# Kernel tuning notes

Measured on AMD Instinct MI355X. Metric: run time of the kernel, lower is better.

The kernel has to match this reference:

```python
import jax, jax.numpy as jnp
import numpy as np
from jax import lax

T = 8        # num_frames
EPS = 1e-5   # batchnorm eps


def conv2d(x, w, b=None, pad=0):
    y = lax.conv_general_dilated(x, w, (1, 1), [(pad, pad), (pad, pad)],
                                 dimension_numbers=('NCHW', 'OIHW', 'NCHW'))
    return y if b is None else y + b[None, :, None, None]


def conv3d(x, w, b, pad=1):
    y = lax.conv_general_dilated(x, w, (1, 1, 1), [(pad, pad)] * 3,
                                 dimension_numbers=('NCDHW', 'OIDHW', 'NCDHW'))
    return y + b[None, :, None, None, None]


def bn(x, g, b, m, v):
    shp = (1, -1) + (1,) * (x.ndim - 2)
    return (x - m.reshape(shp)) * (g.reshape(shp) * lax.rsqrt(v.reshape(shp) + EPS)) + b.reshape(shp)


def deform_conv2d(x, offset, weight, pad):
    # mmcv DeformConv: x (N,C,H,W); offset (N,2*kh*kw,H,W) laid out as (tap, [dy,dx]);
    # weight (O,C,kh,kw); stride 1, zero padding outside sampled via masked bilinear.
    N, C, H, W = x.shape
    O, _, kh, kw = weight.shape
    K = kh * kw
    off = offset.reshape(N, K, 2, H, W)
    ky, kx = jnp.meshgrid(jnp.arange(kh), jnp.arange(kw), indexing='ij')
    # fractional sample coords per (n, tap, out_y, out_x)
    py = (jnp.arange(H)[None, :, None] + (ky.reshape(K) - pad)[:, None, None])[None] + off[:, :, 0]
    px = (jnp.arange(W)[None, None, :] + (kx.reshape(K) - pad)[:, None, None])[None] + off[:, :, 1]
    y0 = jnp.floor(py); x0 = jnp.floor(px)
    ly = py - y0;       lx = px - x0
    y0 = y0.astype(jnp.int32); x0 = x0.astype(jnp.int32)
    xf = x.reshape(N, C, H * W)

    def gather(iy, ix):
        valid = ((iy >= 0) & (iy < H) & (ix >= 0) & (ix < W)).astype(x.dtype)
        lin = jnp.clip(iy, 0, H - 1) * W + jnp.clip(ix, 0, W - 1)   # (N,K,H,W)
        v = jax.vmap(lambda xi, li: xi[:, li])(xf, lin)             # (N,C,K,H,W)
        return v * valid[:, None]

    val = (gather(y0, x0)         * ((1 - ly) * (1 - lx))[:, None]
           + gather(y0, x0 + 1)   * ((1 - ly) * lx)[:, None]
           + gather(y0 + 1, x0)   * (ly * (1 - lx))[:, None]
           + gather(y0 + 1, x0 + 1) * (ly * lx)[:, None])
    return jnp.einsum('nckhw,ock->nohw', val, weight.reshape(O, C, K))


def reference(x, w_down, b_down, bn1_g, bn1_b, bn1_m, bn1_v,
              tconv_w, tconv_b, bnt_g, bnt_b, bnt_m, bnt_v,
              off3_w, off3_b, def3_w, off5_w, off5_b, def5_w,
              conv1_w, conv1_b, bn3_g, bn3_b, bn3_m, bn3_v,
              conv_w, conv_b, bn2_g, bn2_b, bn2_m, bn2_v):
    out = bn(conv2d(x, w_down, b_down), bn1_g, bn1_b, bn1_m, bn1_v)   # (nt, cr, h, w)
    nt, cr, h, w = out.shape
    b = nt // T
    # temporal branch: (b, cr, T, h, w) 3D conv, then mean over time
    t_in = out.reshape(b, T, cr, h, w).transpose(0, 2, 1, 3, 4)
    t_out = bn(conv3d(t_in, tconv_w, tconv_b), bnt_g, bnt_b, bnt_m, bnt_v)
    t_out = t_out.mean(axis=2, keepdims=True).transpose(0, 2, 1, 3, 4)  # (b,1,cr,h,w)
    # motion-difference branches
    o5 = out.reshape(b, T, cr, h, w)
    x_pre = o5[:, :T - 1]
    x_post = o5[:, 1:].reshape(-1, cr, h, w)                           # (b*(T-1), cr, h, w)
    d3 = deform_conv2d(x_post, conv2d(x_post, off3_w, off3_b, pad=1), def3_w, pad=1).reshape(b, T - 1, cr, h, w)
    d5 = deform_conv2d(x_post, conv2d(x_post, off5_w, off5_b, pad=2), def5_w, pad=2).reshape(b, T - 1, cr, h, w)
    mp = lax.reduce_window(x_post, -jnp.inf, lax.max, (1, 1, 3, 3), (1, 1, 1, 1),
                           [(0, 0), (0, 0), (1, 1), (1, 1)])
    d_avg = bn(conv2d(mp, conv1_w, conv1_b), bn3_g, bn3_b, bn3_m, bn3_v).reshape(b, T - 1, cr, h, w)
    diff = jnp.abs(d3 + d5 + d_avg - 3.0 * x_pre)                      # (d3-pre)+(d5-pre)+(avg-pre)
    cat = jnp.concatenate([diff, t_out], axis=1).reshape(-1, cr, h, w) # (nt, cr, h, w)
    gate = bn(conv2d(cat.mean(axis=(2, 3), keepdims=True), conv_w, conv_b),
              bn2_g, bn2_b, bn2_m, bn2_v)
    gate = jax.nn.sigmoid(gate) - 0.5
    return gate * x + x


def setup_inputs():
    key = jax.random.key(0)
    ks = iter(jax.random.split(key, 64))
    C, CR, H, W, B = 256, 64, 28, 28, 8
    NT = B * T
    rn = lambda shape, s: jax.random.normal(next(ks), shape, jnp.float32) * s

    def bnp(c):
        return (1.0 + rn((c,), 0.1), rn((c,), 0.1), rn((c,), 0.1),
                0.5 + jax.random.uniform(next(ks), (c,), jnp.float32))

    inp = {'x': rn((NT, C, H, W), 1.0)}
    inp['w_down'] = rn((CR, C, 1, 1), 0.06); inp['b_down'] = rn((CR,), 0.02)
    inp['bn1_g'], inp['bn1_b'], inp['bn1_m'], inp['bn1_v'] = bnp(CR)
    inp['tconv_w'] = rn((CR, CR, 3, 3, 3), 0.024); inp['tconv_b'] = rn((CR,), 0.02)
    inp['bnt_g'], inp['bnt_b'], inp['bnt_m'], inp['bnt_v'] = bnp(CR)
    inp['off3_w'] = rn((18, CR, 3, 3), 0.01); inp['off3_b'] = rn((18,), 0.01)
    inp['def3_w'] = rn((CR, CR, 3, 3), 0.04)
    inp['off5_w'] = rn((50, CR, 5, 5), 0.005); inp['off5_b'] = rn((50,), 0.01)
    inp['def5_w'] = rn((CR, CR, 5, 5), 0.025)
    inp['conv1_w'] = rn((CR, CR, 1, 1), 0.125); inp['conv1_b'] = rn((CR,), 0.02)
    inp['bn3_g'], inp['bn3_b'], inp['bn3_m'], inp['bn3_v'] = bnp(CR)
    inp['conv_w'] = rn((C, CR, 1, 1), 0.125); inp['conv_b'] = rn((C,), 0.02)
    inp['bn2_g'], inp['bn2_b'], inp['bn2_m'], inp['bn2_v'] = bnp(C)
    return inp
```

## Files before the change

kernel.cpp:

```cpp
#include <hip/hip_runtime.h>
#include <hip/hip_bf16.h>

#define HW 784
#define WD 28
#define NPX (56 * 784)
#define PLANE (56 * 64 * 784)
#define PADPX 1024

using short8 = __attribute__((ext_vector_type(8))) short;
using f32x4  = __attribute__((ext_vector_type(4))) float;

__device__ __forceinline__ float b2f(short s)
{
  return __uint_as_float(((unsigned)(unsigned short)s) << 16);
}

__global__ void k_prep(
    const float* __restrict__ w_down, const float* __restrict__ b_down,
    const float* __restrict__ bn1_g, const float* __restrict__ bn1_b,
    const float* __restrict__ bn1_m, const float* __restrict__ bn1_v,
    const float* __restrict__ tconv_w, const float* __restrict__ tconv_b,
    const float* __restrict__ bnt_g, const float* __restrict__ bnt_b,
    const float* __restrict__ bnt_m, const float* __restrict__ bnt_v,
    const float* __restrict__ off3_w, const float* __restrict__ def3_w,
    const float* __restrict__ off5_w, const float* __restrict__ def5_w,
    const float* __restrict__ conv1_w, const float* __restrict__ conv1_b,
    const float* __restrict__ bn3_g, const float* __restrict__ bn3_b,
    const float* __restrict__ bn3_m, const float* __restrict__ bn3_v,
    const float* __restrict__ conv_w, const float* __restrict__ conv_b,
    const float* __restrict__ bn2_g, const float* __restrict__ bn2_b,
    const float* __restrict__ bn2_m, const float* __restrict__ bn2_v,
    __hip_bfloat16* __restrict__ wdB, float* __restrict__ bias1,
    float* __restrict__ wtT, float* __restrict__ AtBt,
    __hip_bfloat16* __restrict__ wBs3, __hip_bfloat16* __restrict__ wBs5,
    __hip_bfloat16* __restrict__ wBd, __hip_bfloat16* __restrict__ c1B,
    float* __restrict__ B3,
    float* __restrict__ gwT, float* __restrict__ Bg)
{
  const int tid = blockIdx.x * blockDim.x + threadIdx.x;
  const int nth = gridDim.x * blockDim.x;
  for (int i = tid; i < 16 * 4 * 512; i += nth) {
    int j = i & 7; int lane = (i >> 3) & 63;
    int rest = i >> 9; int nt = rest & 3; int ch = rest >> 2;
    int c = (ch & 7) * 32 + ((lane >> 4) << 3) + j;
    int oc = nt * 16 + (lane & 15);
    float s = bn1_g[oc] / sqrtf(bn1_v[oc] + 1e-5f);
    float wv = w_down[oc * 256 + c] * s;
    __hip_bfloat16 h = __float2bfloat16(wv);
    float hi = b2f(*(short*)&h);
    wdB[i] = (ch < 8) ? h : __float2bfloat16(wv - hi);
  }
  for (int i = tid; i < 64; i += nth) {
    float s = bn1_g[i] / sqrtf(bn1_v[i] + 1e-5f);
    bias1[i] = (b_down[i] - bn1_m[i]) * s + bn1_b[i];
  }
  for (int i = tid; i < 192 * 9 * 64; i += nth) {
    int cc = i / (9 * 64); int tap = (i / 64) % 9; int o = i & 63;
    int dt = cc >> 6, c = cc & 63;
    wtT[i] = tconv_w[o * 1728 + c * 27 + dt * 9 + tap];
  }
  for (int i = tid; i < 64; i += nth) {
    float s = bnt_g[i] / sqrtf(bnt_v[i] + 1e-5f);
    AtBt[i] = s * 0.125f;
    AtBt[64 + i] = (tconv_b[i] - bnt_m[i]) * s + bnt_b[i];
  }
  for (int i = tid; i < 9 * 2 * 2 * 512; i += nth) {
    int j = i & 7; int lane = (i >> 3) & 63;
    int rest = i >> 9; int nt = rest % 2; rest /= 2;
    int chunk = rest & 1; int tap = rest >> 1;
    int c = chunk * 32 + ((lane >> 4) << 3) + j;
    int oc = nt * 16 + (lane & 15);
    float v = (oc < 18) ? off3_w[oc * 576 + c * 9 + tap] : 0.f;
    wBs3[i] = __float2bfloat16(v);
  }
  for (int i = tid; i < 25 * 2 * 4 * 512; i += nth) {
    int j = i & 7; int lane = (i >> 3) & 63;
    int rest = i >> 9; int nt = rest % 4; rest /= 4;
    int chunk = rest & 1; int tap = rest >> 1;
    int c = chunk * 32 + ((lane >> 4) << 3) + j;
    int oc = nt * 16 + (lane & 15);
    float v = (oc < 50) ? off5_w[oc * 1600 + c * 25 + tap] : 0.f;
    wBs5[i] = __float2bfloat16(v);
  }
  for (int i = tid; i < 34 * 2 * 4 * 512; i += nth) {
    int j = i & 7; int lane = (i >> 3) & 63;
    int rest = i >> 9; int nt = rest & 3; rest >>= 2;
    int chunk = rest & 1; int tap = rest >> 1;
    int c = chunk * 32 + ((lane >> 4) << 3) + j;
    int oc = nt * 16 + (lane & 15);
    float v = (tap < 9) ? def3_w[oc * 576 + c * 9 + tap]
                        : def5_w[oc * 1600 + c * 25 + (tap - 9)];
    wBd[i] = __float2bfloat16(v);
  }
  for (int i = tid; i < 2 * 4 * 512; i += nth) {
    int j = i & 7; int lane = (i >> 3) & 63;
    int rest = i >> 9; int nt = rest & 3; int chunk = rest >> 2;
    int c = chunk * 32 + ((lane >> 4) << 3) + j;
    int oc = nt * 16 + (lane & 15);
    float s = bn3_g[oc] / sqrtf(bn3_v[oc] + 1e-5f);
    c1B[i] = __float2bfloat16(conv1_w[oc * 64 + c] * s);
  }
  for (int i = tid; i < 64; i += nth) {
    float s = bn3_g[i] / sqrtf(bn3_v[i] + 1e-5f);
    B3[i] = (conv1_b[i] - bn3_m[i]) * s + bn3_b[i];
  }
  for (int i = tid; i < 64 * 256; i += nth) {
    int c = i >> 8, co = i & 255;
    float s = bn2_g[co] / sqrtf(bn2_v[co] + 1e-5f);
    gwT[i] = conv_w[co * 64 + c] * s;
  }
  for (int i = tid; i < 256; i += nth) {
    float s = bn2_g[i] / sqrtf(bn2_v[i] + 1e-5f);
    Bg[i] = (conv_b[i] - bn2_m[i]) * s + bn2_b[i];
  }
}

__global__ void k_zerohalo(float4* __restrict__ p)
{
  const int i = blockIdx.x * 256 + threadIdx.x;
  const int n = i / 1920, rem = i % 1920;
  const int sl = rem >> 3, q = rem & 7;
  int row, col;
  if (sl < 128) {
    int r = sl >> 5;
    row = (r & 1) + ((r >> 1) * 30);
    col = sl & 31;
  } else {
    int t2 = sl - 128;
    row = 2 + (t2 >> 2);
    int qq = t2 & 3;
    col = (qq & 1) + ((qq >> 1) * 30);
  }
  p[((size_t)n * 1024 + row * 32 + col) * 8 + q] =
      make_float4(0.f, 0.f, 0.f, 0.f);
}

__global__ __launch_bounds__(256) void k_down(
    const float* __restrict__ x, const __hip_bfloat16* __restrict__ wdB,
    const float* __restrict__ bias1, float* __restrict__ out,
    __hip_bfloat16* __restrict__ xTbP)
{
  __shared__ float ct[64 * 65];
  const int tid = threadIdx.x;
  const int w = tid >> 6, lane = tid & 63;
  const int quad = lane >> 4, mrow = lane & 15;
  const int gpx = blockIdx.x * 64 + w * 16 + mrow;
  const int f = gpx / HW, px = gpx % HW;
  const float* xp = x + (size_t)f * 256 * HW + px;
  f32x4 acc[4];
#pragma unroll
  for (int nt = 0; nt < 4; nt++) acc[nt] = (f32x4){0.f, 0.f, 0.f, 0.f};

#pragma unroll
  for (int ch = 0; ch < 8; ch++) {
    short8 aH, aL;
#pragma unroll
    for (int j = 0; j < 8; j++) {
      float xv = xp[(ch * 32 + quad * 8 + j) * HW];
      __hip_bfloat16 h = __float2bfloat16(xv);
      aH[j] = *(short*)&h;
      __hip_bfloat16 l = __float2bfloat16(xv - b2f(aH[j]));
      aL[j] = *(short*)&l;
    }
    const short* bwH = (const short*)wdB + (size_t)(ch * 4) * 512 + lane * 8;
    const short* bwL = bwH + 16384;
#pragma unroll
    for (int nt = 0; nt < 4; nt++) {
      short8 bH = *(const short8*)(bwH + nt * 512);
      short8 bL = *(const short8*)(bwL + nt * 512);
      acc[nt] = __builtin_amdgcn_mfma_f32_16x16x32_bf16(aH, bH, acc[nt], 0, 0, 0);
      acc[nt] = __builtin_amdgcn_mfma_f32_16x16x32_bf16(aL, bH, acc[nt], 0, 0, 0);
      acc[nt] = __builtin_amdgcn_mfma_f32_16x16x32_bf16(aH, bL, acc[nt], 0, 0, 0);
    }
  }
#pragma unroll
  for (int nt = 0; nt < 4; nt++) {
    int oc_l = nt * 16 + mrow;
#pragma unroll
    for (int reg = 0; reg < 4; reg++)
      ct[oc_l * 65 + w * 16 + quad * 4 + reg] = acc[nt][reg];
  }
  __syncthreads();
  for (int i = tid; i < 4096; i += 256) {
    int oc = i >> 6, p2 = i & 63;
    int g2 = blockIdx.x * 64 + p2;
    int f2 = g2 / HW, px2 = g2 % HW;
    out[((size_t)f2 * 64 + oc) * HW + px2] = ct[oc * 65 + p2] + bias1[oc];
  }
  for (int i = tid; i < 4096; i += 256) {
    int p2 = i >> 6, oc = i & 63;
    int g2 = blockIdx.x * 64 + p2;
    int f2 = g2 / HW, px2 = g2 % HW;
    if (f2 & 7) {
      int n = (f2 >> 3) * 7 + (f2 & 7) - 1;
      int py = px2 / WD, pxc = px2 % WD;
      __hip_bfloat16 q = __float2bfloat16(ct[oc * 65 + p2] + bias1[oc]);
      ((short*)xTbP)[((size_t)n * PADPX + (py + 2) * 32 + (pxc + 2)) * 64 + oc] =
          *(short*)&q;
    }
  }
}

__global__ void k_makeU(const float* __restrict__ out, float* __restrict__ U)
{
  const int idx = blockIdx.x * 256 + threadIdx.x;
  const int b = idx / (64 * HW);
  const int r = idx % (64 * HW);
  const float* p = out + (size_t)b * 8 * 64 * HW + r;
  float v0 = p[0];
  float s = v0, v = v0;
#pragma unroll
  for (int t = 1; t < 8; t++) { v = p[t * 64 * HW]; s += v; }
  float* u = U + (size_t)b * 192 * HW + r;
  u[0] = s - v;
  u[64 * HW] = s;
  u[128 * HW] = s - v0;
}

__global__ __launch_bounds__(256) void k_tconv(
    const float* __restrict__ U, const float* __restrict__ wtT,
    const float* __restrict__ AtBt, float* __restrict__ t_out)
{
  __shared__ float wl[16 * 9 * 4];
  const int tid = threadIdx.x;
  const int b = blockIdx.x;
  const int px = blockIdx.y * 256 + tid;
  const int o0 = blockIdx.z * 4;
  const bool act = px < HW;
  const int pxe = act ? px : 0;
  const int y = pxe / WD, x = pxe % WD;
  int lin[9]; float msk[9];
#pragma unroll
  for (int t = 0; t < 9; t++) {
    int iy = y + t / 3 - 1, ix = x + t % 3 - 1;
    bool ok = iy >= 0 && iy < WD && ix >= 0 && ix < WD;
    lin[t] = min(max(iy, 0), WD - 1) * WD + min(max(ix, 0), WD - 1);
    msk[t] = ok ? 1.f : 0.f;
  }
  float acc[4];
#pragma unroll
  for (int j = 0; j < 4; j++) acc[j] = 0.f;
  const float* ub = U + (size_t)b * 192 * HW;
  for (int ccb = 0; ccb < 12; ccb++) {
    __syncthreads();
    for (int i = tid; i < 576; i += 256) {
      int ccL = i / 36; int rr = i % 36; int tap = rr >> 2; int j = rr & 3;
      wl[i] = wtT[((ccb * 16 + ccL) * 9 + tap) * 64 + o0 + j];
    }
    __syncthreads();
    for (int ccL = 0; ccL < 16; ccL++) {
      const float* p = ub + (ccb * 16 + ccL) * HW;
      float v[9];
#pragma unroll
      for (int t = 0; t < 9; t++) v[t] = p[lin[t]] * msk[t];
      const float* wr = &wl[ccL * 36];
#pragma unroll
      for (int t = 0; t < 9; t++)
#pragma unroll
        for (int j = 0; j < 4; j++) acc[j] += v[t] * wr[t * 4 + j];
    }
  }
  if (act) {
#pragma unroll
    for (int j = 0; j < 4; j++) {
      int o = o0 + j;
      t_out[(size_t)(b * 64 + o) * HW + px] = acc[j] * AtBt[o] + AtBt[64 + o];
    }
  }
}

template <int KS, int PAD, int OC, int NT>
__global__ __launch_bounds__(256) void k_offconv_mfma(
    const __hip_bfloat16* __restrict__ xTbP,
    const __hip_bfloat16* __restrict__ wBs,
    const float* __restrict__ bias, float* __restrict__ dst)
{
  constexpr int K2 = KS * KS;
  __shared__ float ct[NT * 16 * 65];
  const int tid = threadIdx.x;
  const int w = tid >> 6, lane = tid & 63;
  const int quad = lane >> 4, mrow = lane & 15;
  const int gpx = blockIdx.x * 64 + w * 16 + mrow;
  const int n = gpx / HW, px = gpx % HW;
  const int y = px / WD, x = px % WD;
  const short* xb = (const short*)xTbP + ((size_t)n * PADPX) * 64;
  f32x4 acc[NT];
#pragma unroll
  for (int nt = 0; nt < NT; nt++) acc[nt] = (f32x4){0.f, 0.f, 0.f, 0.f};

  for (int tap = 0; tap < K2; tap++) {
    const short* bw = (const short*)wBs + (size_t)tap * NT * 1024 + lane * 8;
    short8 bf[2 * NT];
#pragma unroll
    for (int q = 0; q < 2 * NT; q++) bf[q] = *(const short8*)(bw + q * 512);
    int ty = tap / KS, tx = tap % KS;
    int sp = (y + ty + (2 - PAD)) * 32 + (x + tx + (2 - PAD));
    const short* ap = xb + sp * 64 + quad * 8;
    short8 a0 = *(const short8*)(ap);
    short8 a1 = *(const short8*)(ap + 32);
#pragma unroll
    for (int nt = 0; nt < NT; nt++)
      acc[nt] = __builtin_amdgcn_mfma_f32_16x16x32_bf16(a0, bf[nt], acc[nt], 0, 0, 0);
#pragma unroll
    for (int nt = 0; nt < NT; nt++)
      acc[nt] = __builtin_amdgcn_mfma_f32_16x16x32_bf16(a1, bf[NT + nt], acc[nt], 0, 0, 0);
  }
#pragma unroll
  for (int nt = 0; nt < NT; nt++) {
    int oc_l = nt * 16 + mrow;
#pragma unroll
    for (int reg = 0; reg < 4; reg++) {
      int pxr = w * 16 + quad * 4 + reg;
      ct[oc_l * 65 + pxr] = acc[nt][reg];
    }
  }
  __syncthreads();
  for (int i = tid; i < OC * 64; i += 256) {
    int oc = i >> 6, p2 = i & 63;
    int g2 = blockIdx.x * 64 + p2;
    int n2 = g2 / HW, px2 = g2 % HW;
    dst[((size_t)n2 * OC + oc) * HW + px2] = ct[oc * 65 + p2] + bias[oc];
  }
}

__global__ __launch_bounds__(448, 6) void k_deform_mfma(
    const __hip_bfloat16* __restrict__ xTbP,
    const float* __restrict__ off3b, const float* __restrict__ off5b,
    const __hip_bfloat16* __restrict__ wBd,
    float* __restrict__ dsum, float* __restrict__ pext)
{
  __shared__ __align__(128) short Fr[784 * 32];
  const int tid = threadIdx.x;
  const int w = tid >> 6, lane = tid & 63;
  const int quad = lane >> 4, mrow = lane & 15;
  const int part = blockIdx.x, n = blockIdx.y, csel = blockIdx.z;

  {
    const short* xb = (const short*)xTbP + (size_t)n * PADPX * 64;
    for (int idx = tid; idx < 784 * 4; idx += 448) {
      int px = idx >> 2, s = idx & 3;
      int py = px / WD, pxc = px % WD;
      float4 v = ((const float4*)(xb + ((py + 2) * 32 + (pxc + 2)) * 64))[csel * 4 + s];
      int slot = (px & ~1) * 4 + ((s ^ ((px >> 1) & 3)) << 1) + (px & 1);
      ((float4*)Fr)[slot] = v;
    }
  }
  __syncthreads();

  const char* F = (const char*)Fr;
  const int px0 = (part * 7 + w) * 16;
  const int pxg = px0 + mrow;
  const int y_g = pxg / WD, x_g = pxg % WD;
  const float* ob3 = off3b + (size_t)n * 18 * HW + pxg;
  const float* ob5 = off5b + (size_t)n * 50 * HW + pxg;

  f32x4 acc[4];
#pragma unroll
  for (int nt = 0; nt < 4; nt++) acc[nt] = (f32x4){0.f, 0.f, 0.f, 0.f};

#pragma unroll 2
  for (int tap = 0; tap < 34; tap++) {
    const short* bw = (const short*)wBd +
        ((size_t)(tap * 2 + csel) * 4) * 512 + lane * 8;
    short8 bfrag[4];
#pragma unroll
    for (int nt = 0; nt < 4; nt++) bfrag[nt] = *(const short8*)(bw + nt * 512);

    int kk, ty, tx, PADl; const float* obp;
    if (tap < 9) { kk = tap; ty = kk / 3; tx = kk % 3; PADl = 1; obp = ob3; }
    else { kk = tap - 9; ty = kk / 5; tx = kk % 5; PADl = 2; obp = ob5; }
    float offy = obp[(2 * kk) * HW];
    float offx = obp[(2 * kk + 1) * HW];
    float py = (float)(y_g + ty - PADl) + offy;
    float pxx = (float)(x_g + tx - PADl) + offx;
    float fy = floorf(py), fx = floorf(pxx);
    int y0 = (int)fy, x0 = (int)fx;
    float ly = py - fy, lx = pxx - fx;
    int y1 = y0 + 1, x1 = x0 + 1;
    float vy0 = (y0 >= 0 && y0 < WD) ? 1.f : 0.f;
    float vy1 = (y1 >= 0 && y1 < WD) ? 1.f : 0.f;
    float vx0 = (x0 >= 0 && x0 < WD) ? 1.f : 0.f;
    float vx1 = (x1 >= 0 && x1 < WD) ? 1.f : 0.f;
    float w00 = (1.f - ly) * (1.f - lx) * vy0 * vx0;
    float w01 = (1.f - ly) * lx * vy0 * vx1;
    float w10 = ly * (1.f - lx) * vy1 * vx0;
    float w11 = ly * lx * vy1 * vx1;
    int cy0 = min(max(y0, 0), WD - 1), cy1 = min(max(y1, 0), WD - 1);
    int cx0 = min(max(x0, 0), WD - 1), cx1 = min(max(x1, 0), WD - 1);
    int r00 = cy0 * WD + cx0, r01 = cy0 * WD + cx1;
    int r10 = cy1 * WD + cx0, r11 = cy1 * WD + cx1;
#define LADDR(r) ((r & ~1) * 64 + (((quad ^ ((r >> 1) & 3))) << 5) + ((r & 1) << 4))
    short8 c00 = *(const short8*)(F + LADDR(r00));
    short8 c01 = *(const short8*)(F + LADDR(r01));
    short8 c10 = *(const short8*)(F + LADDR(r10));
    short8 c11 = *(const short8*)(F + LADDR(r11));
#undef LADDR
    short8 a0;
#pragma unroll
    for (int j = 0; j < 8; j++) {
      float g0 = b2f(c00[j]) * w00 + b2f(c01[j]) * w01 +
                 b2f(c10[j]) * w10 + b2f(c11[j]) * w11;
      __hip_bfloat16 q0 = __float2bfloat16(g0);
      a0[j] = *(short*)&q0;
    }
#pragma unroll
    for (int nt = 0; nt < 4; nt++)
      acc[nt] = __builtin_amdgcn_mfma_f32_16x16x32_bf16(a0, bfrag[nt], acc[nt], 0, 0, 0);
  }

  float* P = csel ? pext : dsum;
#pragma unroll
  for (int nt = 0; nt < 4; nt++)
    *(f32x4*)(P + ((size_t)n * 64 + nt * 16 + mrow) * HW + px0 + quad * 4) =
        acc[nt];
}

__global__ __launch_bounds__(256) void k_davg_diff(
    const float* __restrict__ frames, const __hip_bfloat16* __restrict__ c1B,
    const float* __restrict__ B3, float* __restrict__ dsum,
    const float* __restrict__ pext)
{
  const int tid = threadIdx.x;
  const int w = tid >> 6, lane = tid & 63;
  const int quad = lane >> 4, mrow = lane & 15;
  const int gpx = blockIdx.x * 64 + w * 16 + mrow;
  const int n = gpx / HW, px = gpx % HW;
  const int fpost = (n / 7) * 8 + (n % 7) + 1;
  const int fpre = fpost - 1;
  const int y = px / WD, x = px % WD;
  int lin[9]; bool okm[9];
#pragma unroll
  for (int t2 = 0; t2 < 9; t2++) {
    int iy = y + t2 / 3 - 1, ix = x + t2 % 3 - 1;
    okm[t2] = iy >= 0 && iy < WD && ix >= 0 && ix < WD;
    lin[t2] = min(max(iy, 0), WD - 1) * WD + min(max(ix, 0), WD - 1);
  }
  const float* sb = frames + (size_t)fpost * 64 * HW;
  f32x4 acc[4];
#pragma unroll
  for (int nt = 0; nt < 4; nt++) acc[nt] = (f32x4){0.f, 0.f, 0.f, 0.f};

#pragma unroll
  for (int chunk = 0; chunk < 2; chunk++) {
    short8 aM;
#pragma unroll
    for (int j = 0; j < 8; j++) {
      const float* p = sb + (chunk * 32 + quad * 8 + j) * HW;
      float m = -1e30f;
#pragma unroll
      for (int t2 = 0; t2 < 9; t2++) {
        float v = okm[t2] ? p[lin[t2]] : -1e30f;
        m = fmaxf(m, v);
      }
      __hip_bfloat16 h = __float2bfloat16(m);
      aM[j] = *(short*)&h;
    }
    const short* bw = (const short*)c1B + (size_t)(chunk * 4) * 512 + lane * 8;
#pragma unroll
    for (int nt = 0; nt < 4; nt++) {
      short8 bf = *(const short8*)(bw + nt * 512);
      acc[nt] = __builtin_amdgcn_mfma_f32_16x16x32_bf16(aM, bf, acc[nt], 0, 0, 0);
    }
  }
  const int pxb = (px - mrow) + quad * 4;
#pragma unroll
  for (int nt = 0; nt < 4; nt++) {
    int oc = nt * 16 + mrow;
    size_t base = ((size_t)n * 64 + oc) * HW + pxb;
    f32x4 ds = *(const f32x4*)(dsum + base);
    f32x4 pe = *(const f32x4*)(pext + base);
    f32x4 xp4 = *(const f32x4*)(frames + ((size_t)fpre * 64 + oc) * HW + pxb);
    float b3 = B3[oc];
    f32x4 o;
#pragma unroll
    for (int r = 0; r < 4; r++)
      o[r] = fabsf(ds[r] + pe[r] + acc[nt][r] + b3 - 3.f * xp4[r]);
    *(f32x4*)(dsum + base) = o;
  }
}

__global__ __launch_bounds__(256) void k_gmean(
    const float* __restrict__ dsum, const float* __restrict__ t_out,
    float* __restrict__ gmean)
{
  const int nt = blockIdx.x, cg = blockIdx.y;
  const int c = cg * 4 + (threadIdx.x >> 6), lane = threadIdx.x & 63;
  const int b = nt >> 3, tt = nt & 7;
  const float* p = (tt < 7) ? (dsum + (size_t)((b * 7 + tt) * 64 + c) * HW)
                            : (t_out + (size_t)(b * 64 + c) * HW);
  float s = 0.f;
  for (int i = lane; i < HW; i += 64) s += p[i];
#pragma unroll
  for (int o = 32; o > 0; o >>= 1) s += __shfl_down(s, o, 64);
  if (lane == 0) gmean[nt * 64 + c] = s * (1.f / HW);
}

__global__ __launch_bounds__(256) void k_gate(
    const float* __restrict__ gmean, const float* __restrict__ gwT,
    const float* __restrict__ Bg, float* __restrict__ mult)
{
  __shared__ float gm[64];
  const int nt = blockIdx.x, co = threadIdx.x;
  if (co < 64) gm[co] = gmean[nt * 64 + co];
  __syncthreads();
  float a = 0.f;
#pragma unroll 8
  for (int c = 0; c < 64; c++) a += gm[c] * gwT[c * 256 + co];
  float pre = a + Bg[co];
  mult[nt * 256 + co] = 0.5f + 1.f / (1.f + expf(-pre));
}

__global__ void k_apply(const float* __restrict__ x,
                        const float* __restrict__ mult,
                        float* __restrict__ outp)
{
  const int i = blockIdx.x * 256 + threadIdx.x;
  const int plane = i / 196;
  const float m = mult[plane];
  float4 v = ((const float4*)x)[i];
  v.x *= m; v.y *= m; v.z *= m; v.w *= m;
  ((float4*)outp)[i] = v;
}

extern "C" void kernel_launch(void* const* d_in, const int* in_sizes, int n_in,
                              void* d_out, int out_size, void* d_ws, size_t ws_size,
                              hipStream_t stream)
{
  const float* x       = (const float*)d_in[0];
  const float* w_down  = (const float*)d_in[1];
  const float* b_down  = (const float*)d_in[2];
  const float* bn1_g   = (const float*)d_in[3];
  const float* bn1_b   = (const float*)d_in[4];
  const float* bn1_m   = (const float*)d_in[5];
  const float* bn1_v   = (const float*)d_in[6];
  const float* tconv_w = (const float*)d_in[7];
  const float* tconv_b = (const float*)d_in[8];
  const float* bnt_g   = (const float*)d_in[9];
  const float* bnt_b   = (const float*)d_in[10];
  const float* bnt_m   = (const float*)d_in[11];
  const float* bnt_v   = (const float*)d_in[12];
  const float* off3_w  = (const float*)d_in[13];
  const float* off3_b  = (const float*)d_in[14];
  const float* def3_w  = (const float*)d_in[15];
  const float* off5_w  = (const float*)d_in[16];
  const float* off5_b  = (const float*)d_in[17];
  const float* def5_w  = (const float*)d_in[18];
  const float* conv1_w = (const float*)d_in[19];
  const float* conv1_b = (const float*)d_in[20];
  const float* bn3_g   = (const float*)d_in[21];
  const float* bn3_b   = (const float*)d_in[22];
  const float* bn3_m   = (const float*)d_in[23];
  const float* bn3_v   = (const float*)d_in[24];
  const float* conv_w  = (const float*)d_in[25];
  const float* conv_b  = (const float*)d_in[26];
  const float* bn2_g   = (const float*)d_in[27];
  const float* bn2_b   = (const float*)d_in[28];
  const float* bn2_m   = (const float*)d_in[29];
  const float* bn2_v   = (const float*)d_in[30];

  float* ws = (float*)d_ws;
  float* out_b  = ws; ws += 64 * 64 * HW;
  float* U      = ws; ws += 8 * 192 * HW;
  float* t_out  = ws; ws += 8 * 64 * HW;
  float* off3b  = ws; ws += 56 * 18 * HW;
  float* off5b  = ws; ws += 56 * 50 * HW;
  float* dsum   = ws; ws += PLANE;
  float* pext   = ws; ws += PLANE;
  float* gmean  = ws; ws += 64 * 64;
  float* multb  = ws; ws += 64 * 256;
  float* bias1  = ws; ws += 64;
  float* wtT    = ws; ws += 192 * 9 * 64;
  float* AtBt   = ws; ws += 128;
  float* B3     = ws; ws += 64;
  float* gwT    = ws; ws += 64 * 256;
  float* Bg     = ws; ws += 256;
  __hip_bfloat16* wdB  = (__hip_bfloat16*)ws; ws += 16384;
  __hip_bfloat16* wBs3 = (__hip_bfloat16*)ws; ws += 9216;
  __hip_bfloat16* wBs5 = (__hip_bfloat16*)ws; ws += 51200;
  __hip_bfloat16* wBd  = (__hip_bfloat16*)ws; ws += 69632;
  __hip_bfloat16* c1B  = (__hip_bfloat16*)ws; ws += 2048;
  __hip_bfloat16* xTbP = (__hip_bfloat16*)ws; ws += 56 * PADPX * 64 / 2;

  k_prep<<<256, 256, 0, stream>>>(
      w_down, b_down, bn1_g, bn1_b, bn1_m, bn1_v,
      tconv_w, tconv_b, bnt_g, bnt_b, bnt_m, bnt_v,
      off3_w, def3_w, off5_w, def5_w,
      conv1_w, conv1_b, bn3_g, bn3_b, bn3_m, bn3_v,
      conv_w, conv_b, bn2_g, bn2_b, bn2_m, bn2_v,
      wdB, bias1, wtT, AtBt, wBs3, wBs5, wBd, c1B,
      B3, gwT, Bg);
  k_zerohalo<<<420, 256, 0, stream>>>((float4*)xTbP);

  k_down<<<784, 256, 0, stream>>>(x, wdB, bias1, out_b, xTbP);
  k_makeU<<<1568, 256, 0, stream>>>(out_b, U);
  k_tconv<<<dim3(8, 4, 16), 256, 0, stream>>>(U, wtT, AtBt, t_out);
  k_offconv_mfma<3, 1, 18, 2><<<686, 256, 0, stream>>>(xTbP, wBs3, off3_b, off3b);
  k_offconv_mfma<5, 2, 50, 4><<<686, 256, 0, stream>>>(xTbP, wBs5, off5_b, off5b);
  k_deform_mfma<<<dim3(7, 56, 2), 448, 0, stream>>>(xTbP, off3b, off5b, wBd,
                                                    dsum, pext);
  k_davg_diff<<<686, 256, 0, stream>>>(out_b, c1B, B3, dsum, pext);
  k_gmean<<<dim3(64, 16), 256, 0, stream>>>(dsum, t_out, gmean);
  k_gate<<<64, 256, 0, stream>>>(gmean, gwT, Bg, multb);
  k_apply<<<12544, 256, 0, stream>>>(x, multb, (float*)d_out);
}
```

Before: 403.5 us.

## Compute temporal conv mean via border-masked row sums and fuse gmean into diff kernel

The full 3D temporal conv output was only consumed through its spatial mean, so it is replaced by per-channel 3x3 border-masked window sums (k_rsum) contracted with the weights in a tiny k_tmean kernel. The separate U construction, the tconv kernel and the gmean reduction pass are removed. The davg_diff kernel now reduces its absolute differences directly into gacc with atomics instead of writing them out. The deform kernel's LDS swizzle is also simplified. Atomic float accumulation makes summation order nondeterministic.

```diff
diff --git a/kernel.cpp b/kernel.cpp
--- a/kernel.cpp
+++ b/kernel.cpp
@@ -35,10 +35,12 @@
     __hip_bfloat16* __restrict__ wBs3, __hip_bfloat16* __restrict__ wBs5,
     __hip_bfloat16* __restrict__ wBd, __hip_bfloat16* __restrict__ c1B,
     float* __restrict__ B3,
-    float* __restrict__ gwT, float* __restrict__ Bg)
+    float* __restrict__ gwT, float* __restrict__ Bg,
+    float* __restrict__ gacc)
 {
   const int tid = blockIdx.x * blockDim.x + threadIdx.x;
   const int nth = gridDim.x * blockDim.x;
+  for (int i = tid; i < 64 * 64; i += nth) gacc[i] = 0.f;
   for (int i = tid; i < 16 * 4 * 512; i += nth) {
     int j = i & 7; int lane = (i >> 3) & 63;
     int rest = i >> 9; int nt = rest & 3; int ch = rest >> 2;
@@ -201,71 +203,67 @@
   }
 }
 
-__global__ void k_makeU(const float* __restrict__ out, float* __restrict__ U)
-{
-  const int idx = blockIdx.x * 256 + threadIdx.x;
-  const int b = idx / (64 * HW);
-  const int r = idx % (64 * HW);
-  const float* p = out + (size_t)b * 8 * 64 * HW + r;
-  float v0 = p[0];
-  float s = v0, v = v0;
-#pragma unroll
-  for (int t = 1; t < 8; t++) { v = p[t * 64 * HW]; s += v; }
-  float* u = U + (size_t)b * 192 * HW + r;
-  u[0] = s - v;
-  u[64 * HW] = s;
-  u[128 * HW] = s - v0;
-}
-
-__global__ __launch_bounds__(256) void k_tconv(
-    const float* __restrict__ U, const float* __restrict__ wtT,
-    const float* __restrict__ AtBt, float* __restrict__ t_out)
-{
-  __shared__ float wl[16 * 9 * 4];
-  const int tid = threadIdx.x;
-  const int b = blockIdx.x;
-  const int px = blockIdx.y * 256 + tid;
-  const int o0 = blockIdx.z * 4;
-  const bool act = px < HW;
-  const int pxe = act ? px : 0;
-  const int y = pxe / WD, x = pxe % WD;
-  int lin[9]; float msk[9];
-#pragma unroll
-  for (int t = 0; t < 9; t++) {
-    int iy = y + t / 3 - 1, ix = x + t % 3 - 1;
-    bool ok = iy >= 0 && iy < WD && ix >= 0 && ix < WD;
-    lin[t] = min(max(iy, 0), WD - 1) * WD + min(max(ix, 0), WD - 1);
-    msk[t] = ok ? 1.f : 0.f;
-  }
-  float acc[4];
-#pragma unroll
-  for (int j = 0; j < 4; j++) acc[j] = 0.f;
-  const float* ub = U + (size_t)b * 192 * HW;
-  for (int ccb = 0; ccb < 12; ccb++) {
-    __syncthreads();
-    for (int i = tid; i < 576; i += 256) {
-      int ccL = i / 36; int rr = i % 36; int tap = rr >> 2; int j = rr & 3;
-      wl[i] = wtT[((ccb * 16 + ccL) * 9 + tap) * 64 + o0 + j];
-    }
-    __syncthreads();
-    for (int ccL = 0; ccL < 16; ccL++) {
-      const float* p = ub + (ccb * 16 + ccL) * HW;
-      float v[9];
-#pragma unroll
-      for (int t = 0; t < 9; t++) v[t] = p[lin[t]] * msk[t];
-      const float* wr = &wl[ccL * 36];
-#pragma unroll
-      for (int t = 0; t < 9; t++)
-#pragma unroll
-        for (int j = 0; j < 4; j++) acc[j] += v[t] * wr[t * 4 + j];
-    }
-  }
-  if (act) {
-#pragma unroll
-    for (int j = 0; j < 4; j++) {
-      int o = o0 + j;
-      t_out[(size_t)(b * 64 + o) * HW + px] = acc[j] * AtBt[o] + AtBt[64 + o];
-    }
+__global__ __launch_bounds__(256) void k_rsum(
+    const float* __restrict__ out_b, float* __restrict__ Rm)
+{
+  const int w = threadIdx.x >> 6, lane = threadIdx.x & 63;
+  const int idx = blockIdx.x * 4 + w;
+  const float* p = out_b + (size_t)idx * HW;
+  float a[9];
+#pragma unroll
+  for (int k = 0; k < 9; k++) a[k] = 0.f;
+  for (int i = lane; i < HW; i += 64) {
+    float v = p[i];
+    int row = i / WD, col = i % WD;
+    float mr0 = (row < WD - 1) ? 1.f : 0.f, mr2 = (row > 0) ? 1.f : 0.f;
+    float mc0 = (col < WD - 1) ? 1.f : 0.f, mc2 = (col > 0) ? 1.f : 0.f;
+    float v0 = v * mc0, v2 = v * mc2;
+    a[0] += v0 * mr0; a[1] += v * mr0; a[2] += v2 * mr0;
+    a[3] += v0;       a[4] += v;       a[5] += v2;
+    a[6] += v0 * mr2; a[7] += v * mr2; a[8] += v2 * mr2;
+  }
+#pragma unroll
+  for (int k = 0; k < 9; k++) {
+#pragma unroll
+    for (int o = 32; o > 0; o >>= 1) a[k] += __shfl_down(a[k], o, 64);
+  }
+  if (lane == 0) {
+#pragma unroll
+    for (int k = 0; k < 9; k++) Rm[(size_t)idx * 9 + k] = a[k];
+  }
+}
+
+__global__ __launch_bounds__(256) void k_tmean(
+    const float* __restrict__ Rm, const float* __restrict__ wtT,
+    const float* __restrict__ AtBt, float* __restrict__ gacc)
+{
+  __shared__ float U[3 * 576];
+  __shared__ float ps[4][64];
+  const int b = blockIdx.x, tid = threadIdx.x;
+  for (int i = tid; i < 576; i += 256) {
+    float s = 0.f;
+#pragma unroll
+    for (int t = 0; t < 8; t++) s += Rm[(size_t)(b * 8 + t) * 576 + i];
+    U[0 * 576 + i] = s - Rm[(size_t)(b * 8 + 7) * 576 + i];
+    U[1 * 576 + i] = s;
+    U[2 * 576 + i] = s - Rm[(size_t)(b * 8 + 0) * 576 + i];
+  }
+  __syncthreads();
+  const int oc = tid & 63, part = tid >> 6;
+  float acc = 0.f;
+  for (int dt = 0; dt < 3; dt++)
+    for (int cL = 0; cL < 16; cL++) {
+      int cc = dt * 64 + part * 16 + cL;
+      const float* wr = wtT + (size_t)cc * 9 * 64 + oc;
+      const float* ur = U + dt * 576 + (part * 16 + cL) * 9;
+#pragma unroll
+      for (int t = 0; t < 9; t++) acc += wr[t * 64] * ur[t];
+    }
+  ps[part][oc] = acc;
+  __syncthreads();
+  if (tid < 64) {
+    float tot = ps[0][tid] + ps[1][tid] + ps[2][tid] + ps[3][tid];
+    gacc[(b * 8 + 7) * 64 + tid] = AtBt[tid] * tot + 784.f * AtBt[64 + tid];
   }
 }
 
@@ -329,7 +327,7 @@
     const __hip_bfloat16* __restrict__ wBd,
     float* __restrict__ dsum, float* __restrict__ pext)
 {
-  __shared__ __align__(128) short Fr[784 * 32];
+  __shared__ __align__(16) short Fr[784 * 32];
   const int tid = threadIdx.x;
   const int w = tid >> 6, lane = tid & 63;
   const int quad = lane >> 4, mrow = lane & 15;
@@ -341,8 +339,7 @@
       int px = idx >> 2, s = idx & 3;
       int py = px / WD, pxc = px % WD;
       float4 v = ((const float4*)(xb + ((py + 2) * 32 + (pxc + 2)) * 64))[csel * 4 + s];
-      int slot = (px & ~1) * 4 + ((s ^ ((px >> 1) & 3)) << 1) + (px & 1);
-      ((float4*)Fr)[slot] = v;
+      ((float4*)Fr)[px * 4 + (s ^ (px & 3))] = v;
     }
   }
   __syncthreads();
@@ -389,12 +386,10 @@
     int cx0 = min(max(x0, 0), WD - 1), cx1 = min(max(x1, 0), WD - 1);
     int r00 = cy0 * WD + cx0, r01 = cy0 * WD + cx1;
     int r10 = cy1 * WD + cx0, r11 = cy1 * WD + cx1;
-#define LADDR(r) ((r & ~1) * 64 + (((quad ^ ((r >> 1) & 3))) << 5) + ((r & 1) << 4))
-    short8 c00 = *(const short8*)(F + LADDR(r00));
-    short8 c01 = *(const short8*)(F + LADDR(r01));
-    short8 c10 = *(const short8*)(F + LADDR(r10));
-    short8 c11 = *(const short8*)(F + LADDR(r11));
-#undef LADDR
+    short8 c00 = *(const short8*)(F + r00 * 64 + ((quad ^ (r00 & 3)) << 4));
+    short8 c01 = *(const short8*)(F + r01 * 64 + ((quad ^ (r01 & 3)) << 4));
+    short8 c10 = *(const short8*)(F + r10 * 64 + ((quad ^ (r10 & 3)) << 4));
+    short8 c11 = *(const short8*)(F + r11 * 64 + ((quad ^ (r11 & 3)) << 4));
     short8 a0;
 #pragma unroll
     for (int j = 0; j < 8; j++) {
@@ -417,8 +412,8 @@
 
 __global__ __launch_bounds__(256) void k_davg_diff(
     const float* __restrict__ frames, const __hip_bfloat16* __restrict__ c1B,
-    const float* __restrict__ B3, float* __restrict__ dsum,
-    const float* __restrict__ pext)
+    const float* __restrict__ B3, const float* __restrict__ dsum,
+    const float* __restrict__ pext, float* __restrict__ gacc)
 {
   const int tid = threadIdx.x;
   const int w = tid >> 6, lane = tid & 63;
@@ -463,6 +458,7 @@
     }
   }
   const int pxb = (px - mrow) + quad * 4;
+  const int gi = ((n / 7) * 8 + (n % 7)) * 64;
 #pragma unroll
   for (int nt = 0; nt < 4; nt++) {
     int oc = nt * 16 + mrow;
@@ -471,37 +467,23 @@
     f32x4 pe = *(const f32x4*)(pext + base);
     f32x4 xp4 = *(const f32x4*)(frames + ((size_t)fpre * 64 + oc) * HW + pxb);
     float b3 = B3[oc];
-    f32x4 o;
+    float s = 0.f;
 #pragma unroll
     for (int r = 0; r < 4; r++)
-      o[r] = fabsf(ds[r] + pe[r] + acc[nt][r] + b3 - 3.f * xp4[r]);
-    *(f32x4*)(dsum + base) = o;
-  }
-}
-
-__global__ __launch_bounds__(256) void k_gmean(
-    const float* __restrict__ dsum, const float* __restrict__ t_out,
-    float* __restrict__ gmean)
-{
-  const int nt = blockIdx.x, cg = blockIdx.y;
-  const int c = cg * 4 + (threadIdx.x >> 6), lane = threadIdx.x & 63;
-  const int b = nt >> 3, tt = nt & 7;
-  const float* p = (tt < 7) ? (dsum + (size_t)((b * 7 + tt) * 64 + c) * HW)
-                            : (t_out + (size_t)(b * 64 + c) * HW);
-  float s = 0.f;
-  for (int i = lane; i < HW; i += 64) s += p[i];
-#pragma unroll
-  for (int o = 32; o > 0; o >>= 1) s += __shfl_down(s, o, 64);
-  if (lane == 0) gmean[nt * 64 + c] = s * (1.f / HW);
+      s += fabsf(ds[r] + pe[r] + acc[nt][r] + b3 - 3.f * xp4[r]);
+    s += __shfl_xor(s, 16, 64);
+    s += __shfl_xor(s, 32, 64);
+    if (quad == 0) atomicAdd(&gacc[gi + oc], s);
+  }
 }
 
 __global__ __launch_bounds__(256) void k_gate(
-    const float* __restrict__ gmean, const float* __restrict__ gwT,
+    const float* __restrict__ gacc, const float* __restrict__ gwT,
     const float* __restrict__ Bg, float* __restrict__ mult)
 {
   __shared__ float gm[64];
   const int nt = blockIdx.x, co = threadIdx.x;
-  if (co < 64) gm[co] = gmean[nt * 64 + co];
+  if (co < 64) gm[co] = gacc[nt * 64 + co] * (1.f / 784.f);
   __syncthreads();
   float a = 0.f;
 #pragma unroll 8
@@ -560,13 +542,12 @@
 
   float* ws = (float*)d_ws;
   float* out_b  = ws; ws += 64 * 64 * HW;
-  float* U      = ws; ws += 8 * 192 * HW;
-  float* t_out  = ws; ws += 8 * 64 * HW;
   float* off3b  = ws; ws += 56 * 18 * HW;
   float* off5b  = ws; ws += 56 * 50 * HW;
   float* dsum   = ws; ws += PLANE;
   float* pext   = ws; ws += PLANE;
-  float* gmean  = ws; ws += 64 * 64;
+  float* Rm     = ws; ws += 64 * 64 * 9;
+  float* gacc   = ws; ws += 64 * 64;
   float* multb  = ws; ws += 64 * 256;
   float* bias1  = ws; ws += 64;
   float* wtT    = ws; ws += 192 * 9 * 64;
@@ -588,18 +569,17 @@
       conv1_w, conv1_b, bn3_g, bn3_b, bn3_m, bn3_v,
       conv_w, conv_b, bn2_g, bn2_b, bn2_m, bn2_v,
       wdB, bias1, wtT, AtBt, wBs3, wBs5, wBd, c1B,
-      B3, gwT, Bg);
+      B3, gwT, Bg, gacc);
   k_zerohalo<<<420, 256, 0, stream>>>((float4*)xTbP);
 
   k_down<<<784, 256, 0, stream>>>(x, wdB, bias1, out_b, xTbP);
-  k_makeU<<<1568, 256, 0, stream>>>(out_b, U);
-  k_tconv<<<dim3(8, 4, 16), 256, 0, stream>>>(U, wtT, AtBt, t_out);
+  k_rsum<<<1024, 256, 0, stream>>>(out_b, Rm);
+  k_tmean<<<8, 256, 0, stream>>>(Rm, wtT, AtBt, gacc);
   k_offconv_mfma<3, 1, 18, 2><<<686, 256, 0, stream>>>(xTbP, wBs3, off3_b, off3b);
   k_offconv_mfma<5, 2, 50, 4><<<686, 256, 0, stream>>>(xTbP, wBs5, off5_b, off5b);
   k_deform_mfma<<<dim3(7, 56, 2), 448, 0, stream>>>(xTbP, off3b, off5b, wBd,
                                                     dsum, pext);
-  k_davg_diff<<<686, 256, 0, stream>>>(out_b, c1B, B3, dsum, pext);
-  k_gmean<<<dim3(64, 16), 256, 0, stream>>>(dsum, t_out, gmean);
-  k_gate<<<64, 256, 0, stream>>>(gmean, gwT, Bg, multb);
+  k_davg_diff<<<686, 256, 0, stream>>>(out_b, c1B, B3, dsum, pext, gacc);
+  k_gate<<<64, 256, 0, stream>>>(gacc, gwT, Bg, multb);
   k_apply<<<12544, 256, 0, stream>>>(x, multb, (float*)d_out);
 }
```

Result: faster. 346.6 us (-14.1%).
